# Optimization experiments

Hardware: AMD Instinct MI355X
Metric: run time of the kernel (lower is better)

The kernel has to match this reference:

```python
import jax, jax.numpy as jnp
import numpy as np

B, H, W, C = 1, 56, 56, 96
DI = 192          # d_inner = ssm_ratio * hidden_dim
N  = 16           # d_state
DR = 6            # dt_rank = ceil(96/16)
K  = 4            # cross-scan directions
MH = 384          # mlp hidden = 4*C
L  = H * W


def _ln(x, g, b):
    m = x.mean(-1, keepdims=True)
    v = ((x - m) ** 2).mean(-1, keepdims=True)
    return (x - m) * jax.lax.rsqrt(v + 1e-5) * g + b


def setup_inputs() -> dict:
    key = jax.random.key(0)
    ks = jax.random.split(key, 12)
    r = lambda i, shape, s=0.02: jax.random.normal(ks[i], shape, jnp.float32) * s
    # S4D-real init for A_logs: log(1..N) tiled over K*DI channels
    A_logs = jnp.log(jnp.tile(jnp.arange(1, N + 1, dtype=jnp.float32)[None, :], (K * DI, 1)))
    return dict(
        x=jax.random.normal(ks[0], (B, H, W, C), jnp.float32),
        norm_g=jnp.ones((C,)), norm_b=jnp.zeros((C,)),
        in_proj_w=r(1, (C, 2 * DI)),
        conv_w=r(2, (3, 3, 1, DI)), conv_b=jnp.zeros((DI,)),
        x_proj_w=r(3, (K, DR + 2 * N, DI)),
        dt_projs_w=r(4, (K, DI, DR), 0.1), dt_projs_b=r(5, (K, DI), 0.1),
        A_logs=A_logs, Ds=jnp.ones((K * DI,)),
        out_norm_g=jnp.ones((DI,)), out_norm_b=jnp.zeros((DI,)),
        out_proj_w=r(6, (DI, C)),
        norm2_g=jnp.ones((C,)), norm2_b=jnp.zeros((C,)),
        fc1_w=r(7, (C, MH)), fc1_b=jnp.zeros((MH,)),
        fc2_w=r(8, (MH, C)), fc2_b=jnp.zeros((C,)),
    )


def _ss2d(x, in_proj_w, conv_w, conv_b, x_proj_w, dt_projs_w, dt_projs_b,
          A_logs, Ds, out_norm_g, out_norm_b, out_proj_w):
    xz = x @ in_proj_w                                  # (B,H,W,2*DI)
    xx, z = xz[..., :DI], xz[..., DI:]
    z = jax.nn.silu(z)
    xx = jax.lax.conv_general_dilated(
        xx, conv_w, (1, 1), 'SAME',
        dimension_numbers=('NHWC', 'HWIO', 'NHWC'),
        feature_group_count=DI) + conv_b               # depthwise 3x3
    xx = jax.nn.silu(xx)
    # cross-scan: row-major, col-major, and their reverses -> (B,K,DI,L)
    xd = jnp.transpose(xx, (0, 3, 1, 2)).reshape(B, DI, L)
    xt = jnp.transpose(xx, (0, 3, 2, 1)).reshape(B, DI, L)
    xs = jnp.stack([xd, xt, xd[..., ::-1], xt[..., ::-1]], 1)
    xdbl = jnp.einsum('bkdl,kcd->bkcl', xs, x_proj_w)
    dts, Bs, Cs = xdbl[:, :, :DR], xdbl[:, :, DR:DR + N], xdbl[:, :, DR + N:]
    dts = jnp.einsum('bkrl,kdr->bkdl', dts, dt_projs_w)
    dts = jax.nn.softplus(dts + dt_projs_b[None, :, :, None])      # (B,K,DI,L)
    A = -jnp.exp(A_logs).reshape(K, DI, N)
    # selective scan as first-order linear recurrence h_t = a_t*h_{t-1} + b_t
    a = jnp.exp(dts[..., None] * A[None, :, :, None, :])           # (B,K,DI,L,N)
    b = dts[..., None] * jnp.swapaxes(Bs, -1, -2)[:, :, None] * xs[..., None]
    def comb(c1, c2):
        a1, b1 = c1
        a2, b2 = c2
        return a1 * a2, a2 * b1 + b2
    _, hs = jax.lax.associative_scan(comb, (a, b), axis=3)         # (B,K,DI,L,N)
    ys = jnp.einsum('bkdln,bknl->bkdl', hs, Cs) + Ds.reshape(K, DI)[None, :, :, None] * xs
    # cross-merge: un-flip, un-transpose, sum the 4 directions
    yrow = ys[:, 0] + ys[:, 2, :, ::-1]
    ycol = ys[:, 1] + ys[:, 3, :, ::-1]
    y = yrow + jnp.transpose(ycol.reshape(B, DI, W, H), (0, 1, 3, 2)).reshape(B, DI, L)
    y = jnp.transpose(y.reshape(B, DI, H, W), (0, 2, 3, 1))        # (B,H,W,DI)
    y = _ln(y, out_norm_g, out_norm_b) * z
    return y @ out_proj_w


def reference(x, norm_g, norm_b, in_proj_w, conv_w, conv_b, x_proj_w,
              dt_projs_w, dt_projs_b, A_logs, Ds, out_norm_g, out_norm_b,
              out_proj_w, norm2_g, norm2_b, fc1_w, fc1_b, fc2_w, fc2_b):
    x = x + _ss2d(_ln(x, norm_g, norm_b), in_proj_w, conv_w, conv_b, x_proj_w,
                  dt_projs_w, dt_projs_b, A_logs, Ds, out_norm_g, out_norm_b, out_proj_w)
    h = _ln(x, norm2_g, norm2_b)
    x = x + (jax.nn.gelu(h @ fc1_w + fc1_b) @ fc2_w + fc2_b)
    return x
```

## Files before the change

kernel.cpp:

```cpp
#include <hip/hip_runtime.h>
#include <math.h>

constexpr int cH = 56, cW = 56, cC = 96, cDI = 192, cN = 16, cDR = 6, cK = 4, cMH = 384;
constexpr int cL = cH * cW;
constexpr int cNC = 98;
constexpr int cCH = 32;
constexpr float LOG2E = 1.44269504088896340736f;

__device__ __forceinline__ float fast_exp2(float x) { return __builtin_amdgcn_exp2f(x); }
__device__ __forceinline__ float siluf(float x) { return x / (1.f + expf(-x)); }
__device__ __forceinline__ float geluf(float x) {
    float x3 = x * x * x;
    return 0.5f * x * (1.f + tanhf(0.7978845608028654f * (x + 0.044715f * x3)));
}

template <int ACT, bool HASB>
__global__ __launch_bounds__(256) void gemm_ln_tile(
    const float* __restrict__ A, const float* __restrict__ g, const float* __restrict__ b,
    const float* __restrict__ B, const float* __restrict__ bias,
    float* __restrict__ C, int M, int Nn) {
    __shared__ float As[64][100];
    __shared__ float Bs2[32][32];
    __shared__ float gB[96], bB[96], rowM[64], rowR[64];
    int tid = threadIdx.x;
    int row0 = blockIdx.y * 64;
    int n0 = blockIdx.x * 32;
    if (tid < 96) { gB[tid] = g[tid]; bB[tid] = b[tid]; }
#pragma unroll
    for (int t = 0; t < 6; t++) {
        int f = tid + t * 256;
        int ar = f / 24, ac4 = (f % 24) * 4;
        const float4 v = *reinterpret_cast<const float4*>(A + (size_t)(row0 + ar) * 96 + ac4);
        *reinterpret_cast<float4*>(&As[ar][ac4]) = v;
    }
    __syncthreads();
    {
        int row = tid >> 2, q = tid & 3;
        float s = 0.f, sq = 0.f;
#pragma unroll
        for (int c = 0; c < 24; c++) {
            float v = As[row][q * 24 + c];
            s += v; sq += v * v;
        }
        s += __shfl_xor(s, 1); sq += __shfl_xor(sq, 1);
        s += __shfl_xor(s, 2); sq += __shfl_xor(sq, 2);
        if (q == 0) {
            float m = s * (1.f / 96.f);
            float var = sq * (1.f / 96.f) - m * m;
            rowM[row] = m;
            rowR[row] = rsqrtf(var + 1e-5f);
        }
    }
    __syncthreads();
    for (int i = tid; i < 64 * 96; i += 256) {
        int r = i / 96, c = i % 96;
        As[r][c] = (As[r][c] - rowM[r]) * rowR[r] * gB[c] + bB[c];
    }
    __syncthreads();
    int tx = tid & 15, ty = tid >> 4;
    float acc[4][2] = {{0.f, 0.f}, {0.f, 0.f}, {0.f, 0.f}, {0.f, 0.f}};
#pragma unroll
    for (int kt = 0; kt < 3; kt++) {
        {
            int br = tid >> 3, bc = (tid & 7) * 4;
            const float4 v = *reinterpret_cast<const float4*>(
                B + (size_t)(kt * 32 + br) * Nn + n0 + bc);
            *reinterpret_cast<float4*>(&Bs2[br][bc]) = v;
        }
        __syncthreads();
#pragma unroll
        for (int k4 = 0; k4 < 8; k4++) {
            float4 a0 = *reinterpret_cast<float4*>(&As[ty * 4 + 0][kt * 32 + k4 * 4]);
            float4 a1 = *reinterpret_cast<float4*>(&As[ty * 4 + 1][kt * 32 + k4 * 4]);
            float4 a2 = *reinterpret_cast<float4*>(&As[ty * 4 + 2][kt * 32 + k4 * 4]);
            float4 a3 = *reinterpret_cast<float4*>(&As[ty * 4 + 3][kt * 32 + k4 * 4]);
            float2 b0 = *reinterpret_cast<float2*>(&Bs2[k4 * 4 + 0][tx * 2]);
            float2 b1 = *reinterpret_cast<float2*>(&Bs2[k4 * 4 + 1][tx * 2]);
            float2 b2 = *reinterpret_cast<float2*>(&Bs2[k4 * 4 + 2][tx * 2]);
            float2 b3 = *reinterpret_cast<float2*>(&Bs2[k4 * 4 + 3][tx * 2]);
            acc[0][0] = fmaf(a0.x, b0.x, acc[0][0]); acc[0][1] = fmaf(a0.x, b0.y, acc[0][1]);
            acc[1][0] = fmaf(a1.x, b0.x, acc[1][0]); acc[1][1] = fmaf(a1.x, b0.y, acc[1][1]);
            acc[2][0] = fmaf(a2.x, b0.x, acc[2][0]); acc[2][1] = fmaf(a2.x, b0.y, acc[2][1]);
            acc[3][0] = fmaf(a3.x, b0.x, acc[3][0]); acc[3][1] = fmaf(a3.x, b0.y, acc[3][1]);
            acc[0][0] = fmaf(a0.y, b1.x, acc[0][0]); acc[0][1] = fmaf(a0.y, b1.y, acc[0][1]);
            acc[1][0] = fmaf(a1.y, b1.x, acc[1][0]); acc[1][1] = fmaf(a1.y, b1.y, acc[1][1]);
            acc[2][0] = fmaf(a2.y, b1.x, acc[2][0]); acc[2][1] = fmaf(a2.y, b1.y, acc[2][1]);
            acc[3][0] = fmaf(a3.y, b1.x, acc[3][0]); acc[3][1] = fmaf(a3.y, b1.y, acc[3][1]);
            acc[0][0] = fmaf(a0.z, b2.x, acc[0][0]); acc[0][1] = fmaf(a0.z, b2.y, acc[0][1]);
            acc[1][0] = fmaf(a1.z, b2.x, acc[1][0]); acc[1][1] = fmaf(a1.z, b2.y, acc[1][1]);
            acc[2][0] = fmaf(a2.z, b2.x, acc[2][0]); acc[2][1] = fmaf(a2.z, b2.y, acc[2][1]);
            acc[3][0] = fmaf(a3.z, b2.x, acc[3][0]); acc[3][1] = fmaf(a3.z, b2.y, acc[3][1]);
            acc[0][0] = fmaf(a0.w, b3.x, acc[0][0]); acc[0][1] = fmaf(a0.w, b3.y, acc[0][1]);
            acc[1][0] = fmaf(a1.w, b3.x, acc[1][0]); acc[1][1] = fmaf(a1.w, b3.y, acc[1][1]);
            acc[2][0] = fmaf(a2.w, b3.x, acc[2][0]); acc[2][1] = fmaf(a2.w, b3.y, acc[2][1]);
            acc[3][0] = fmaf(a3.w, b3.x, acc[3][0]); acc[3][1] = fmaf(a3.w, b3.y, acc[3][1]);
        }
        __syncthreads();
    }
    int cc = n0 + tx * 2;
    float bx_ = 0.f, by_ = 0.f;
    if (HASB) { bx_ = bias[cc]; by_ = bias[cc + 1]; }
#pragma unroll
    for (int i = 0; i < 4; i++) {
        int rr = row0 + ty * 4 + i;
        float v0 = acc[i][0], v1 = acc[i][1];
        if (HASB) { v0 += bx_; v1 += by_; }
        if (ACT == 1) { v0 = geluf(v0); v1 = geluf(v1); }
        float2 o; o.x = v0; o.y = v1;
        *reinterpret_cast<float2*>(C + (size_t)rr * Nn + cc) = o;
    }
}

template <int ACT, bool HASB, bool HASR>
__global__ __launch_bounds__(256) void gemm_tile_kernel(
    const float* __restrict__ A, const float* __restrict__ B,
    const float* __restrict__ bias, const float* __restrict__ res,
    float* __restrict__ C, int M, int Nn, int Kk) {
    __shared__ float As[64][36];
    __shared__ float Bs[32][32];
    int tid = threadIdx.x;
    int tx = tid & 15;
    int ty = tid >> 4;
    int row0 = blockIdx.y * 64;
    int n0 = blockIdx.x * 32;
    float acc[4][2] = {{0.f, 0.f}, {0.f, 0.f}, {0.f, 0.f}, {0.f, 0.f}};
    int nt = Kk >> 5;
    for (int kt = 0; kt < nt; kt++) {
#pragma unroll
        for (int t = 0; t < 2; t++) {
            int f = tid + t * 256;
            int ar = f >> 3, ac = (f & 7) * 4;
            const float4 v = *reinterpret_cast<const float4*>(
                A + (size_t)(row0 + ar) * Kk + kt * 32 + ac);
            *reinterpret_cast<float4*>(&As[ar][ac]) = v;
        }
        {
            int br = tid >> 3, bc = (tid & 7) * 4;
            const float4 v = *reinterpret_cast<const float4*>(
                B + (size_t)(kt * 32 + br) * Nn + n0 + bc);
            *reinterpret_cast<float4*>(&Bs[br][bc]) = v;
        }
        __syncthreads();
#pragma unroll
        for (int k4 = 0; k4 < 8; k4++) {
            float4 a0 = *reinterpret_cast<float4*>(&As[ty * 4 + 0][k4 * 4]);
            float4 a1 = *reinterpret_cast<float4*>(&As[ty * 4 + 1][k4 * 4]);
            float4 a2 = *reinterpret_cast<float4*>(&As[ty * 4 + 2][k4 * 4]);
            float4 a3 = *reinterpret_cast<float4*>(&As[ty * 4 + 3][k4 * 4]);
            float2 b0 = *reinterpret_cast<float2*>(&Bs[k4 * 4 + 0][tx * 2]);
            float2 b1 = *reinterpret_cast<float2*>(&Bs[k4 * 4 + 1][tx * 2]);
            float2 b2 = *reinterpret_cast<float2*>(&Bs[k4 * 4 + 2][tx * 2]);
            float2 b3 = *reinterpret_cast<float2*>(&Bs[k4 * 4 + 3][tx * 2]);
            acc[0][0] = fmaf(a0.x, b0.x, acc[0][0]); acc[0][1] = fmaf(a0.x, b0.y, acc[0][1]);
            acc[1][0] = fmaf(a1.x, b0.x, acc[1][0]); acc[1][1] = fmaf(a1.x, b0.y, acc[1][1]);
            acc[2][0] = fmaf(a2.x, b0.x, acc[2][0]); acc[2][1] = fmaf(a2.x, b0.y, acc[2][1]);
            acc[3][0] = fmaf(a3.x, b0.x, acc[3][0]); acc[3][1] = fmaf(a3.x, b0.y, acc[3][1]);
            acc[0][0] = fmaf(a0.y, b1.x, acc[0][0]); acc[0][1] = fmaf(a0.y, b1.y, acc[0][1]);
            acc[1][0] = fmaf(a1.y, b1.x, acc[1][0]); acc[1][1] = fmaf(a1.y, b1.y, acc[1][1]);
            acc[2][0] = fmaf(a2.y, b1.x, acc[2][0]); acc[2][1] = fmaf(a2.y, b1.y, acc[2][1]);
            acc[3][0] = fmaf(a3.y, b1.x, acc[3][0]); acc[3][1] = fmaf(a3.y, b1.y, acc[3][1]);
            acc[0][0] = fmaf(a0.z, b2.x, acc[0][0]); acc[0][1] = fmaf(a0.z, b2.y, acc[0][1]);
            acc[1][0] = fmaf(a1.z, b2.x, acc[1][0]); acc[1][1] = fmaf(a1.z, b2.y, acc[1][1]);
            acc[2][0] = fmaf(a2.z, b2.x, acc[2][0]); acc[2][1] = fmaf(a2.z, b2.y, acc[2][1]);
            acc[3][0] = fmaf(a3.z, b2.x, acc[3][0]); acc[3][1] = fmaf(a3.z, b2.y, acc[3][1]);
            acc[0][0] = fmaf(a0.w, b3.x, acc[0][0]); acc[0][1] = fmaf(a0.w, b3.y, acc[0][1]);
            acc[1][0] = fmaf(a1.w, b3.x, acc[1][0]); acc[1][1] = fmaf(a1.w, b3.y, acc[1][1]);
            acc[2][0] = fmaf(a2.w, b3.x, acc[2][0]); acc[2][1] = fmaf(a2.w, b3.y, acc[2][1]);
            acc[3][0] = fmaf(a3.w, b3.x, acc[3][0]); acc[3][1] = fmaf(a3.w, b3.y, acc[3][1]);
        }
        __syncthreads();
    }
    int cc = n0 + tx * 2;
    float bx_ = 0.f, by_ = 0.f;
    if (HASB) { bx_ = bias[cc]; by_ = bias[cc + 1]; }
#pragma unroll
    for (int i = 0; i < 4; i++) {
        int rr = row0 + ty * 4 + i;
        float v0 = acc[i][0], v1 = acc[i][1];
        if (HASB) { v0 += bx_; v1 += by_; }
        if (ACT == 1) { v0 = geluf(v0); v1 = geluf(v1); }
        if (HASR) {
            const float2 r2 = *reinterpret_cast<const float2*>(res + (size_t)rr * Nn + cc);
            v0 += r2.x; v1 += r2.y;
        }
        float2 o; o.x = v0; o.y = v1;
        *reinterpret_cast<float2*>(C + (size_t)rr * Nn + cc) = o;
    }
}

__global__ void conv_silu_kernel(const float* __restrict__ xz, const float* __restrict__ cw,
                                 const float* __restrict__ cb, float* __restrict__ out) {
    int idx = blockIdx.x * 256 + threadIdx.x;
    if (idx >= cL * cDI) return;
    int d = idx % cDI;
    int l = idx / cDI;
    int h = l / cW, w = l % cW;
    float s = cb[d];
#pragma unroll
    for (int dh = 0; dh < 3; dh++) {
        int hh = h + dh - 1;
        if (hh < 0 || hh >= cH) continue;
#pragma unroll
        for (int dw = 0; dw < 3; dw++) {
            int w2 = w + dw - 1;
            if (w2 < 0 || w2 >= cW) continue;
            s = fmaf(xz[(size_t)(hh * cW + w2) * (2 * cDI) + d], cw[(dh * 3 + dw) * cDI + d], s);
        }
    }
    out[idx] = siluf(s);
}

__global__ void proj_kernel(const float* __restrict__ xconv, const float* __restrict__ xpw,
                            const float* __restrict__ dtw, const float* __restrict__ dtb,
                            float* __restrict__ dtT, float* __restrict__ Bsout,
                            float* __restrict__ Csout) {
    __shared__ float XS[16 * 196];
    __shared__ float DTS[6 * 16];
    __shared__ float DTW[cDI * cDR];
    int k = blockIdx.y;
    int p0 = blockIdx.x * 16;
    int tid = threadIdx.x;
    for (int i = tid; i < cDI * cDR; i += 256) DTW[i] = dtw[k * cDI * cDR + i];
    for (int idx = tid; idx < 16 * cDI; idx += 256) {
        int p = idx / cDI, d = idx % cDI;
        int j = p0 + p;
        int jj = (k >= 2) ? (cL - 1 - j) : j;
        int rrow = (k & 1) ? ((jj % cH) * cW + (jj / cH)) : jj;
        XS[p * 196 + d] = xconv[(size_t)rrow * cDI + d];
    }
    __syncthreads();
    for (int o = tid; o < 38 * 16; o += 256) {
        int c = o >> 4, p = o & 15;
        const float* wr = xpw + (size_t)(k * 38 + c) * cDI;
        const float* xr = XS + p * 196;
        float a0 = 0.f, a1 = 0.f, a2 = 0.f, a3 = 0.f;
#pragma unroll 4
        for (int d = 0; d < cDI; d += 4) {
            const float4 wv = *reinterpret_cast<const float4*>(wr + d);
            const float4 xv = *reinterpret_cast<const float4*>(xr + d);
            a0 = fmaf(wv.x, xv.x, a0);
            a1 = fmaf(wv.y, xv.y, a1);
            a2 = fmaf(wv.z, xv.z, a2);
            a3 = fmaf(wv.w, xv.w, a3);
        }
        float s = (a0 + a1) + (a2 + a3);
        if (c < 6) DTS[c * 16 + p] = s;
        else if (c < 22) Bsout[(size_t)(k * cL + p0 + p) * cN + (c - 6)] = s;
        else Csout[(size_t)(k * cL + p0 + p) * cN + (c - 22)] = s;
    }
    __syncthreads();
    for (int o = tid; o < cDI * 16; o += 256) {
        int d = o % cDI, p = o / cDI;
        float s = dtb[k * cDI + d];
#pragma unroll
        for (int r = 0; r < cDR; r++) s = fmaf(DTW[d * cDR + r], DTS[r * 16 + p], s);
        float sp = (s > 20.f) ? s : log1pf(expf(s));
        dtT[(size_t)(k * cL + p0 + p) * cDI + d] = sp;
    }
}

__device__ __forceinline__ void walker_init(int k, int j0, int& r, int& dr) {
    if (k == 0) { r = j0; dr = 1; }
    else if (k == 1) { r = (j0 % cH) * cW + (j0 / cH); dr = cW; }
    else if (k == 2) { r = cL - 1 - j0; dr = -1; }
    else { int jp = cL - 1 - j0; r = (jp % cH) * cW + (jp / cH); dr = -cW; }
}
__device__ __forceinline__ void walker_step(int& r, int dr) {
    r += dr;
    if (r >= cL) r -= cL - 1;
    else if (r < 0) r += cL - 1;
}

__global__ __launch_bounds__(192) void scan1_kernel(
    const float* __restrict__ dtT, const float* __restrict__ Bs,
    const float* __restrict__ xconv, const float* __restrict__ Alogs,
    float* __restrict__ carryP, float* __restrict__ carryH) {
    int c = blockIdx.x % cNC;
    int k = blockIdx.x / cNC;
    int d = threadIdx.x;
    int kd = k * cDI + d;
    int j0 = c * cCH;
    __shared__ float BS[cCH * cN];
    for (int i = threadIdx.x; i < cCH * cN; i += 192)
        BS[i] = Bs[(size_t)(k * cL + j0) * cN + i];
    float An2[cN];
#pragma unroll
    for (int n = 0; n < cN; n++)
        An2[n] = -fast_exp2(Alogs[kd * cN + n] * LOG2E) * LOG2E;
    int r, dr;
    walker_init(k, j0, r, dr);
    __syncthreads();
    float h[cN];
#pragma unroll
    for (int n = 0; n < cN; n++) h[n] = 0.f;
    float S = 0.f;
    const float* dtp = dtT + (size_t)(k * cL + j0) * cDI + d;
    for (int i = 0; i < cCH; i++) {
        float dt = dtp[(size_t)i * cDI];
        float xv = xconv[r * cDI + d];
        walker_step(r, dr);
        float dtx = dt * xv;
        S += dt;
        const float4 b0 = *reinterpret_cast<const float4*>(&BS[i * cN + 0]);
        const float4 b1 = *reinterpret_cast<const float4*>(&BS[i * cN + 4]);
        const float4 b2 = *reinterpret_cast<const float4*>(&BS[i * cN + 8]);
        const float4 b3 = *reinterpret_cast<const float4*>(&BS[i * cN + 12]);
        float bb[cN] = {b0.x, b0.y, b0.z, b0.w, b1.x, b1.y, b1.z, b1.w,
                        b2.x, b2.y, b2.z, b2.w, b3.x, b3.y, b3.z, b3.w};
#pragma unroll
        for (int n = 0; n < cN; n++) {
            float a = fast_exp2(An2[n] * dt);
            h[n] = fmaf(a, h[n], bb[n] * dtx);
        }
    }
    size_t cb = (size_t)(kd * cNC + c) * cN;
#pragma unroll
    for (int n = 0; n < cN; n++) {
        carryH[cb + n] = h[n];
        carryP[cb + n] = fast_exp2(An2[n] * S);
    }
}

__global__ void scan2_kernel(const float* __restrict__ carryP, const float* __restrict__ carryH,
                             float* __restrict__ hin) {
    int gid = blockIdx.x * 256 + threadIdx.x;
    if (gid >= cK * cDI * cN) return;
    int kd = gid / cN, n = gid % cN;
    float h = 0.f;
    for (int c = 0; c < cNC; c++) {
        size_t idxc = (size_t)(kd * cNC + c) * cN + n;
        hin[idxc] = h;
        h = fmaf(carryP[idxc], h, carryH[idxc]);
    }
}

__global__ __launch_bounds__(192) void scan3_kernel(
    const float* __restrict__ dtT, const float* __restrict__ Bs,
    const float* __restrict__ Cs, const float* __restrict__ xconv,
    const float* __restrict__ Alogs, const float* __restrict__ Ds,
    const float* __restrict__ hin, float* __restrict__ ysS) {
    int c = blockIdx.x % cNC;
    int k = blockIdx.x / cNC;
    int d = threadIdx.x;
    int kd = k * cDI + d;
    int j0 = c * cCH;
    __shared__ float BS[cCH * cN];
    __shared__ float CS[cCH * cN];
    for (int i = threadIdx.x; i < cCH * cN; i += 192) {
        BS[i] = Bs[(size_t)(k * cL + j0) * cN + i];
        CS[i] = Cs[(size_t)(k * cL + j0) * cN + i];
    }
    float An2[cN];
#pragma unroll
    for (int n = 0; n < cN; n++)
        An2[n] = -fast_exp2(Alogs[kd * cN + n] * LOG2E) * LOG2E;
    float Dv = Ds[kd];
    int r, dr;
    walker_init(k, j0, r, dr);
    float h[cN];
    size_t cb = (size_t)(kd * cNC + c) * cN;
#pragma unroll
    for (int n = 0; n < cN; n++) h[n] = hin[cb + n];
    __syncthreads();
    const float* dtp = dtT + (size_t)(k * cL + j0) * cDI + d;
    float* yp = ysS + (size_t)(k * cL + j0) * cDI + d;
    for (int i = 0; i < cCH; i++) {
        float dt = dtp[(size_t)i * cDI];
        float xv = xconv[r * cDI + d];
        walker_step(r, dr);
        float dtx = dt * xv;
        const float4 b0 = *reinterpret_cast<const float4*>(&BS[i * cN + 0]);
        const float4 b1 = *reinterpret_cast<const float4*>(&BS[i * cN + 4]);
        const float4 b2 = *reinterpret_cast<const float4*>(&BS[i * cN + 8]);
        const float4 b3 = *reinterpret_cast<const float4*>(&BS[i * cN + 12]);
        float bb[cN] = {b0.x, b0.y, b0.z, b0.w, b1.x, b1.y, b1.z, b1.w,
                        b2.x, b2.y, b2.z, b2.w, b3.x, b3.y, b3.z, b3.w};
        const float4 c0 = *reinterpret_cast<const float4*>(&CS[i * cN + 0]);
        const float4 c1 = *reinterpret_cast<const float4*>(&CS[i * cN + 4]);
        const float4 c2 = *reinterpret_cast<const float4*>(&CS[i * cN + 8]);
        const float4 c3 = *reinterpret_cast<const float4*>(&CS[i * cN + 12]);
        float cc[cN] = {c0.x, c0.y, c0.z, c0.w, c1.x, c1.y, c1.z, c1.w,
                        c2.x, c2.y, c2.z, c2.w, c3.x, c3.y, c3.z, c3.w};
        float y0 = 0.f, y1 = 0.f, y2 = 0.f, y3 = 0.f;
#pragma unroll
        for (int n = 0; n < cN; n += 4) {
            float a0 = fast_exp2(An2[n + 0] * dt);
            float a1 = fast_exp2(An2[n + 1] * dt);
            float a2 = fast_exp2(An2[n + 2] * dt);
            float a3 = fast_exp2(An2[n + 3] * dt);
            h[n + 0] = fmaf(a0, h[n + 0], bb[n + 0] * dtx);
            h[n + 1] = fmaf(a1, h[n + 1], bb[n + 1] * dtx);
            h[n + 2] = fmaf(a2, h[n + 2], bb[n + 2] * dtx);
            h[n + 3] = fmaf(a3, h[n + 3], bb[n + 3] * dtx);
            y0 = fmaf(h[n + 0], cc[n + 0], y0);
            y1 = fmaf(h[n + 1], cc[n + 1], y1);
            y2 = fmaf(h[n + 2], cc[n + 2], y2);
            y3 = fmaf(h[n + 3], cc[n + 3], y3);
        }
        yp[(size_t)i * cDI] = (y0 + y1) + (y2 + y3) + Dv * xv;
    }
}

__global__ void lnout_kernel(const float* __restrict__ ysS, const float* __restrict__ xz,
                             const float* __restrict__ g, const float* __restrict__ b,
                             float* __restrict__ ymul) {
    int wid = threadIdx.x >> 6, lane = threadIdx.x & 63;
    int l = blockIdx.x * 4 + wid;
    if (l >= cL) return;
    int h_ = l / cW, w_ = l % cW;
    int lc = w_ * cH + h_;
    float v[3];
    float s = 0.f, sq = 0.f;
#pragma unroll
    for (int j = 0; j < 3; j++) {
        int d = lane + j * 64;
        float t = ysS[(size_t)(0 * cL + l) * cDI + d] +
                  ysS[(size_t)(1 * cL + lc) * cDI + d] +
                  ysS[(size_t)(2 * cL + (cL - 1 - l)) * cDI + d] +
                  ysS[(size_t)(3 * cL + (cL - 1 - lc)) * cDI + d];
        v[j] = t;
        s += t;
        sq += t * t;
    }
#pragma unroll
    for (int off = 32; off; off >>= 1) {
        s += __shfl_xor(s, off, 64);
        sq += __shfl_xor(sq, off, 64);
    }
    float m = s * (1.f / cDI);
    float var = sq * (1.f / cDI) - m * m;
    float rstd = rsqrtf(var + 1e-5f);
#pragma unroll
    for (int j = 0; j < 3; j++) {
        int d = lane + j * 64;
        float z = xz[(size_t)l * (2 * cDI) + cDI + d];
        ymul[(size_t)l * cDI + d] = ((v[j] - m) * rstd * g[d] + b[d]) * siluf(z);
    }
}

extern "C" void kernel_launch(void* const* d_in, const int* in_sizes, int n_in,
                              void* d_out, int out_size, void* d_ws, size_t ws_size,
                              hipStream_t stream) {
    const float* x         = (const float*)d_in[0];
    const float* norm_g    = (const float*)d_in[1];
    const float* norm_b    = (const float*)d_in[2];
    const float* in_proj_w = (const float*)d_in[3];
    const float* conv_w    = (const float*)d_in[4];
    const float* conv_b    = (const float*)d_in[5];
    const float* x_proj_w  = (const float*)d_in[6];
    const float* dt_projs_w= (const float*)d_in[7];
    const float* dt_projs_b= (const float*)d_in[8];
    const float* A_logs    = (const float*)d_in[9];
    const float* Ds        = (const float*)d_in[10];
    const float* out_norm_g= (const float*)d_in[11];
    const float* out_norm_b= (const float*)d_in[12];
    const float* out_proj_w= (const float*)d_in[13];
    const float* norm2_g   = (const float*)d_in[14];
    const float* norm2_b   = (const float*)d_in[15];
    const float* fc1_w     = (const float*)d_in[16];
    const float* fc1_b     = (const float*)d_in[17];
    const float* fc2_w     = (const float*)d_in[18];
    const float* fc2_b     = (const float*)d_in[19];

    float* ws = (float*)d_ws;
    float* xz     = ws;
    float* xconv  = ws + 1204224;
    float* dtT    = ws + 1806336;
    float* Bs     = ws + 4214784;
    float* Cs     = ws + 4415488;
    float* hin    = ws + 4616192;
    float* cP     = ws + 5820416;
    float* cHh    = ws + 7024640;
    float* ysS    = ws + 8228864;
    float* x1     = ws + 10637312;
    float* ymul   = xconv;
    float* hm     = xz;
    float* out    = (float*)d_out;

    gemm_ln_tile<0, false><<<dim3(384 / 32, cL / 64), 256, 0, stream>>>(
        x, norm_g, norm_b, in_proj_w, nullptr, xz, cL, 2 * cDI);
    conv_silu_kernel<<<(cL * cDI) / 256, 256, 0, stream>>>(xz, conv_w, conv_b, xconv);
    proj_kernel<<<dim3(cL / 16, cK), 256, 0, stream>>>(xconv, x_proj_w, dt_projs_w,
                                                       dt_projs_b, dtT, Bs, Cs);
    scan1_kernel<<<cK * cNC, 192, 0, stream>>>(dtT, Bs, xconv, A_logs, cP, cHh);
    scan2_kernel<<<(cK * cDI * cN + 255) / 256, 256, 0, stream>>>(cP, cHh, hin);
    scan3_kernel<<<cK * cNC, 192, 0, stream>>>(dtT, Bs, Cs, xconv, A_logs, Ds, hin, ysS);
    lnout_kernel<<<cL / 4, 256, 0, stream>>>(ysS, xz, out_norm_g, out_norm_b, ymul);
    gemm_tile_kernel<0, false, true><<<dim3(96 / 32, cL / 64), 256, 0, stream>>>(
        ymul, out_proj_w, nullptr, x, x1, cL, cC, cDI);
    gemm_ln_tile<1, true><<<dim3(384 / 32, cL / 64), 256, 0, stream>>>(
        x1, norm2_g, norm2_b, fc1_w, fc1_b, hm, cL, cMH);
    gemm_tile_kernel<0, true, true><<<dim3(96 / 32, cL / 64), 256, 0, stream>>>(
        hm, fc2_w, fc2_b, x1, out, cL, cC, cMH);
}
```

Before: 163.0 us.

## Fuse projection with chunk scan, pre-permute cross-scan inputs, fuse out-norm with out_proj

The conv kernel now writes the four cross-scan orderings of its output directly, so later stages read them contiguously instead of walking strided indices. The x_proj/dt_proj kernel now also runs the first chunked scan pass on 16-step chunks from shared memory, which removes the separate scan1 launch and its re-reads of dt, B and x. Scan3 reads hin at every other chunk to match the finer chunking. The out-norm/gating kernel is fused with the out_proj GEMM plus residual, so the gated activations no longer go to global memory. The costs are four times the xs writes, twice as many carries for scan2, and a simple non-tiled GEMM in the fused out_proj.

```diff
diff --git a/kernel.cpp b/kernel.cpp
--- a/kernel.cpp
+++ b/kernel.cpp
@@ -3,8 +3,10 @@
 
 constexpr int cH = 56, cW = 56, cC = 96, cDI = 192, cN = 16, cDR = 6, cK = 4, cMH = 384;
 constexpr int cL = cH * cW;
-constexpr int cNC = 98;
-constexpr int cCH = 32;
+constexpr int cNC1 = 196;
+constexpr int cCH1 = 16;
+constexpr int cNC3 = 98;
+constexpr int cCH3 = 32;
 constexpr float LOG2E = 1.44269504088896340736f;
 
 __device__ __forceinline__ float fast_exp2(float x) { return __builtin_amdgcn_exp2f(x); }
@@ -189,7 +191,7 @@
 }
 
 __global__ void conv_silu_kernel(const float* __restrict__ xz, const float* __restrict__ cw,
-                                 const float* __restrict__ cb, float* __restrict__ out) {
+                                 const float* __restrict__ cb, float* __restrict__ xsS) {
     int idx = blockIdx.x * 256 + threadIdx.x;
     if (idx >= cL * cDI) return;
     int d = idx % cDI;
@@ -207,31 +209,38 @@
             s = fmaf(xz[(size_t)(hh * cW + w2) * (2 * cDI) + d], cw[(dh * 3 + dw) * cDI + d], s);
         }
     }
-    out[idx] = siluf(s);
-}
-
-__global__ void proj_kernel(const float* __restrict__ xconv, const float* __restrict__ xpw,
-                            const float* __restrict__ dtw, const float* __restrict__ dtb,
-                            float* __restrict__ dtT, float* __restrict__ Bsout,
-                            float* __restrict__ Csout) {
+    s = siluf(s);
+    int j1 = w * cH + h;
+    xsS[(size_t)(0 * cL + l) * cDI + d] = s;
+    xsS[(size_t)(1 * cL + j1) * cDI + d] = s;
+    xsS[(size_t)(2 * cL + (cL - 1 - l)) * cDI + d] = s;
+    xsS[(size_t)(3 * cL + (cL - 1 - j1)) * cDI + d] = s;
+}
+
+__global__ __launch_bounds__(256) void proj_scan1_kernel(
+    const float* __restrict__ xsS, const float* __restrict__ xpw,
+    const float* __restrict__ dtw, const float* __restrict__ dtb,
+    const float* __restrict__ Alogs,
+    float* __restrict__ dtT, float* __restrict__ Bsout, float* __restrict__ Csout,
+    float* __restrict__ carryP, float* __restrict__ carryH) {
     __shared__ float XS[16 * 196];
     __shared__ float DTS[6 * 16];
     __shared__ float DTW[cDI * cDR];
+    __shared__ float BSL[16 * 16];
+    __shared__ float DTL[16 * cDI];
     int k = blockIdx.y;
-    int p0 = blockIdx.x * 16;
+    int c = blockIdx.x;
+    int p0 = c * 16;
     int tid = threadIdx.x;
     for (int i = tid; i < cDI * cDR; i += 256) DTW[i] = dtw[k * cDI * cDR + i];
     for (int idx = tid; idx < 16 * cDI; idx += 256) {
         int p = idx / cDI, d = idx % cDI;
-        int j = p0 + p;
-        int jj = (k >= 2) ? (cL - 1 - j) : j;
-        int rrow = (k & 1) ? ((jj % cH) * cW + (jj / cH)) : jj;
-        XS[p * 196 + d] = xconv[(size_t)rrow * cDI + d];
+        XS[p * 196 + d] = xsS[(size_t)(k * cL + p0 + p) * cDI + d];
     }
     __syncthreads();
     for (int o = tid; o < 38 * 16; o += 256) {
-        int c = o >> 4, p = o & 15;
-        const float* wr = xpw + (size_t)(k * 38 + c) * cDI;
+        int cc = o >> 4, p = o & 15;
+        const float* wr = xpw + (size_t)(k * 38 + cc) * cDI;
         const float* xr = XS + p * 196;
         float a0 = 0.f, a1 = 0.f, a2 = 0.f, a3 = 0.f;
 #pragma unroll 4
@@ -244,9 +253,11 @@
             a3 = fmaf(wv.w, xv.w, a3);
         }
         float s = (a0 + a1) + (a2 + a3);
-        if (c < 6) DTS[c * 16 + p] = s;
-        else if (c < 22) Bsout[(size_t)(k * cL + p0 + p) * cN + (c - 6)] = s;
-        else Csout[(size_t)(k * cL + p0 + p) * cN + (c - 22)] = s;
+        if (cc < 6) DTS[cc * 16 + p] = s;
+        else if (cc < 22) {
+            BSL[p * 16 + (cc - 6)] = s;
+            Bsout[(size_t)(k * cL + p0 + p) * cN + (cc - 6)] = s;
+        } else Csout[(size_t)(k * cL + p0 + p) * cN + (cc - 22)] = s;
     }
     __syncthreads();
     for (int o = tid; o < cDI * 16; o += 256) {
@@ -255,69 +266,44 @@
 #pragma unroll
         for (int r = 0; r < cDR; r++) s = fmaf(DTW[d * cDR + r], DTS[r * 16 + p], s);
         float sp = (s > 20.f) ? s : log1pf(expf(s));
+        DTL[p * cDI + d] = sp;
         dtT[(size_t)(k * cL + p0 + p) * cDI + d] = sp;
     }
-}
-
-__device__ __forceinline__ void walker_init(int k, int j0, int& r, int& dr) {
-    if (k == 0) { r = j0; dr = 1; }
-    else if (k == 1) { r = (j0 % cH) * cW + (j0 / cH); dr = cW; }
-    else if (k == 2) { r = cL - 1 - j0; dr = -1; }
-    else { int jp = cL - 1 - j0; r = (jp % cH) * cW + (jp / cH); dr = -cW; }
-}
-__device__ __forceinline__ void walker_step(int& r, int dr) {
-    r += dr;
-    if (r >= cL) r -= cL - 1;
-    else if (r < 0) r += cL - 1;
-}
-
-__global__ __launch_bounds__(192) void scan1_kernel(
-    const float* __restrict__ dtT, const float* __restrict__ Bs,
-    const float* __restrict__ xconv, const float* __restrict__ Alogs,
-    float* __restrict__ carryP, float* __restrict__ carryH) {
-    int c = blockIdx.x % cNC;
-    int k = blockIdx.x / cNC;
-    int d = threadIdx.x;
-    int kd = k * cDI + d;
-    int j0 = c * cCH;
-    __shared__ float BS[cCH * cN];
-    for (int i = threadIdx.x; i < cCH * cN; i += 192)
-        BS[i] = Bs[(size_t)(k * cL + j0) * cN + i];
-    float An2[cN];
-#pragma unroll
-    for (int n = 0; n < cN; n++)
-        An2[n] = -fast_exp2(Alogs[kd * cN + n] * LOG2E) * LOG2E;
-    int r, dr;
-    walker_init(k, j0, r, dr);
-    __syncthreads();
-    float h[cN];
-#pragma unroll
-    for (int n = 0; n < cN; n++) h[n] = 0.f;
-    float S = 0.f;
-    const float* dtp = dtT + (size_t)(k * cL + j0) * cDI + d;
-    for (int i = 0; i < cCH; i++) {
-        float dt = dtp[(size_t)i * cDI];
-        float xv = xconv[r * cDI + d];
-        walker_step(r, dr);
-        float dtx = dt * xv;
-        S += dt;
-        const float4 b0 = *reinterpret_cast<const float4*>(&BS[i * cN + 0]);
-        const float4 b1 = *reinterpret_cast<const float4*>(&BS[i * cN + 4]);
-        const float4 b2 = *reinterpret_cast<const float4*>(&BS[i * cN + 8]);
-        const float4 b3 = *reinterpret_cast<const float4*>(&BS[i * cN + 12]);
-        float bb[cN] = {b0.x, b0.y, b0.z, b0.w, b1.x, b1.y, b1.z, b1.w,
-                        b2.x, b2.y, b2.z, b2.w, b3.x, b3.y, b3.z, b3.w};
+    __syncthreads();
+    if (tid < cDI) {
+        int d = tid;
+        int kd = k * cDI + d;
+        float An2[cN];
+#pragma unroll
+        for (int n = 0; n < cN; n++)
+            An2[n] = -fast_exp2(Alogs[kd * cN + n] * LOG2E) * LOG2E;
+        float h[cN];
+#pragma unroll
+        for (int n = 0; n < cN; n++) h[n] = 0.f;
+        float S = 0.f;
+        for (int p = 0; p < cCH1; p++) {
+            float dt = DTL[p * cDI + d];
+            float xv = XS[p * 196 + d];
+            float dtx = dt * xv;
+            S += dt;
+            const float4 b0 = *reinterpret_cast<const float4*>(&BSL[p * 16 + 0]);
+            const float4 b1 = *reinterpret_cast<const float4*>(&BSL[p * 16 + 4]);
+            const float4 b2 = *reinterpret_cast<const float4*>(&BSL[p * 16 + 8]);
+            const float4 b3 = *reinterpret_cast<const float4*>(&BSL[p * 16 + 12]);
+            float bb[cN] = {b0.x, b0.y, b0.z, b0.w, b1.x, b1.y, b1.z, b1.w,
+                            b2.x, b2.y, b2.z, b2.w, b3.x, b3.y, b3.z, b3.w};
+#pragma unroll
+            for (int n = 0; n < cN; n++) {
+                float a = fast_exp2(An2[n] * dt);
+                h[n] = fmaf(a, h[n], bb[n] * dtx);
+            }
+        }
+        size_t cb = (size_t)(kd * cNC1 + c) * cN;
 #pragma unroll
         for (int n = 0; n < cN; n++) {
-            float a = fast_exp2(An2[n] * dt);
-            h[n] = fmaf(a, h[n], bb[n] * dtx);
-        }
-    }
-    size_t cb = (size_t)(kd * cNC + c) * cN;
-#pragma unroll
-    for (int n = 0; n < cN; n++) {
-        carryH[cb + n] = h[n];
-        carryP[cb + n] = fast_exp2(An2[n] * S);
+            carryH[cb + n] = h[n];
+            carryP[cb + n] = fast_exp2(An2[n] * S);
+        }
     }
 }
 
@@ -327,8 +313,8 @@
     if (gid >= cK * cDI * cN) return;
     int kd = gid / cN, n = gid % cN;
     float h = 0.f;
-    for (int c = 0; c < cNC; c++) {
-        size_t idxc = (size_t)(kd * cNC + c) * cN + n;
+    for (int c = 0; c < cNC1; c++) {
+        size_t idxc = (size_t)(kd * cNC1 + c) * cN + n;
         hin[idxc] = h;
         h = fmaf(carryP[idxc], h, carryH[idxc]);
     }
@@ -336,17 +322,17 @@
 
 __global__ __launch_bounds__(192) void scan3_kernel(
     const float* __restrict__ dtT, const float* __restrict__ Bs,
-    const float* __restrict__ Cs, const float* __restrict__ xconv,
+    const float* __restrict__ Cs, const float* __restrict__ xsS,
     const float* __restrict__ Alogs, const float* __restrict__ Ds,
     const float* __restrict__ hin, float* __restrict__ ysS) {
-    int c = blockIdx.x % cNC;
-    int k = blockIdx.x / cNC;
+    int c3 = blockIdx.x % cNC3;
+    int k = blockIdx.x / cNC3;
     int d = threadIdx.x;
     int kd = k * cDI + d;
-    int j0 = c * cCH;
-    __shared__ float BS[cCH * cN];
-    __shared__ float CS[cCH * cN];
-    for (int i = threadIdx.x; i < cCH * cN; i += 192) {
+    int j0 = c3 * cCH3;
+    __shared__ float BS[cCH3 * cN];
+    __shared__ float CS[cCH3 * cN];
+    for (int i = threadIdx.x; i < cCH3 * cN; i += 192) {
         BS[i] = Bs[(size_t)(k * cL + j0) * cN + i];
         CS[i] = Cs[(size_t)(k * cL + j0) * cN + i];
     }
@@ -355,19 +341,17 @@
     for (int n = 0; n < cN; n++)
         An2[n] = -fast_exp2(Alogs[kd * cN + n] * LOG2E) * LOG2E;
     float Dv = Ds[kd];
-    int r, dr;
-    walker_init(k, j0, r, dr);
     float h[cN];
-    size_t cb = (size_t)(kd * cNC + c) * cN;
-#pragma unroll
-    for (int n = 0; n < cN; n++) h[n] = hin[cb + n];
+    size_t hb = (size_t)(kd * cNC1 + 2 * c3) * cN;
+#pragma unroll
+    for (int n = 0; n < cN; n++) h[n] = hin[hb + n];
     __syncthreads();
     const float* dtp = dtT + (size_t)(k * cL + j0) * cDI + d;
+    const float* xsp = xsS + (size_t)(k * cL + j0) * cDI + d;
     float* yp = ysS + (size_t)(k * cL + j0) * cDI + d;
-    for (int i = 0; i < cCH; i++) {
+    for (int i = 0; i < cCH3; i++) {
         float dt = dtp[(size_t)i * cDI];
-        float xv = xconv[r * cDI + d];
-        walker_step(r, dr);
+        float xv = xsp[(size_t)i * cDI];
         float dtx = dt * xv;
         const float4 b0 = *reinterpret_cast<const float4*>(&BS[i * cN + 0]);
         const float4 b1 = *reinterpret_cast<const float4*>(&BS[i * cN + 4]);
@@ -378,9 +362,9 @@
         const float4 c0 = *reinterpret_cast<const float4*>(&CS[i * cN + 0]);
         const float4 c1 = *reinterpret_cast<const float4*>(&CS[i * cN + 4]);
         const float4 c2 = *reinterpret_cast<const float4*>(&CS[i * cN + 8]);
-        const float4 c3 = *reinterpret_cast<const float4*>(&CS[i * cN + 12]);
+        const float4 c3v = *reinterpret_cast<const float4*>(&CS[i * cN + 12]);
         float cc[cN] = {c0.x, c0.y, c0.z, c0.w, c1.x, c1.y, c1.z, c1.w,
-                        c2.x, c2.y, c2.z, c2.w, c3.x, c3.y, c3.z, c3.w};
+                        c2.x, c2.y, c2.z, c2.w, c3v.x, c3v.y, c3v.z, c3v.w};
         float y0 = 0.f, y1 = 0.f, y2 = 0.f, y3 = 0.f;
 #pragma unroll
         for (int n = 0; n < cN; n += 4) {
@@ -401,40 +385,74 @@
     }
 }
 
-__global__ void lnout_kernel(const float* __restrict__ ysS, const float* __restrict__ xz,
-                             const float* __restrict__ g, const float* __restrict__ b,
-                             float* __restrict__ ymul) {
-    int wid = threadIdx.x >> 6, lane = threadIdx.x & 63;
-    int l = blockIdx.x * 4 + wid;
-    if (l >= cL) return;
-    int h_ = l / cW, w_ = l % cW;
-    int lc = w_ * cH + h_;
-    float v[3];
-    float s = 0.f, sq = 0.f;
-#pragma unroll
-    for (int j = 0; j < 3; j++) {
-        int d = lane + j * 64;
-        float t = ysS[(size_t)(0 * cL + l) * cDI + d] +
+__global__ __launch_bounds__(256) void lnout_proj_kernel(
+    const float* __restrict__ ysS, const float* __restrict__ xz,
+    const float* __restrict__ g, const float* __restrict__ b,
+    const float* __restrict__ W, const float* __restrict__ resx,
+    float* __restrict__ x1) {
+    __shared__ float YL[8][200];
+    __shared__ float gB[cDI], bB[cDI], rowM[8], rowR[8];
+    int tid = threadIdx.x;
+    int l0 = blockIdx.x * 8;
+    if (tid < cDI) { gB[tid] = g[tid]; bB[tid] = b[tid]; }
+#pragma unroll
+    for (int t = 0; t < 6; t++) {
+        int idx = tid + t * 256;
+        int r = idx / cDI, d = idx % cDI;
+        int l = l0 + r;
+        int h_ = l / cW, w_ = l % cW;
+        int lc = w_ * cH + h_;
+        float v = ysS[(size_t)(0 * cL + l) * cDI + d] +
                   ysS[(size_t)(1 * cL + lc) * cDI + d] +
                   ysS[(size_t)(2 * cL + (cL - 1 - l)) * cDI + d] +
                   ysS[(size_t)(3 * cL + (cL - 1 - lc)) * cDI + d];
-        v[j] = t;
-        s += t;
-        sq += t * t;
-    }
-#pragma unroll
-    for (int off = 32; off; off >>= 1) {
-        s += __shfl_xor(s, off, 64);
-        sq += __shfl_xor(sq, off, 64);
-    }
-    float m = s * (1.f / cDI);
-    float var = sq * (1.f / cDI) - m * m;
-    float rstd = rsqrtf(var + 1e-5f);
-#pragma unroll
-    for (int j = 0; j < 3; j++) {
-        int d = lane + j * 64;
+        YL[r][d] = v;
+    }
+    __syncthreads();
+    {
+        int r = tid >> 5, sg = tid & 31;
+        float s = 0.f, sq = 0.f;
+#pragma unroll
+        for (int m = 0; m < 6; m++) {
+            float v = YL[r][sg + 32 * m];
+            s += v; sq += v * v;
+        }
+        s += __shfl_xor(s, 1, 32); sq += __shfl_xor(sq, 1, 32);
+        s += __shfl_xor(s, 2, 32); sq += __shfl_xor(sq, 2, 32);
+        s += __shfl_xor(s, 4, 32); sq += __shfl_xor(sq, 4, 32);
+        s += __shfl_xor(s, 8, 32); sq += __shfl_xor(sq, 8, 32);
+        s += __shfl_xor(s, 16, 32); sq += __shfl_xor(sq, 16, 32);
+        if (sg == 0) {
+            float m = s * (1.f / cDI);
+            float var = sq * (1.f / cDI) - m * m;
+            rowM[r] = m;
+            rowR[r] = rsqrtf(var + 1e-5f);
+        }
+    }
+    __syncthreads();
+#pragma unroll
+    for (int t = 0; t < 6; t++) {
+        int idx = tid + t * 256;
+        int r = idx / cDI, d = idx % cDI;
+        int l = l0 + r;
         float z = xz[(size_t)l * (2 * cDI) + cDI + d];
-        ymul[(size_t)l * cDI + d] = ((v[j] - m) * rstd * g[d] + b[d]) * siluf(z);
+        YL[r][d] = ((YL[r][d] - rowM[r]) * rowR[r] * gB[d] + bB[d]) * siluf(z);
+    }
+    __syncthreads();
+#pragma unroll
+    for (int t = 0; t < 3; t++) {
+        int o = tid + t * 256;
+        int r = o / 96, cc = o % 96;
+        float a0 = 0.f, a1 = 0.f, a2 = 0.f, a3 = 0.f;
+#pragma unroll 4
+        for (int kk = 0; kk < cDI; kk += 4) {
+            a0 = fmaf(YL[r][kk + 0], W[(size_t)(kk + 0) * 96 + cc], a0);
+            a1 = fmaf(YL[r][kk + 1], W[(size_t)(kk + 1) * 96 + cc], a1);
+            a2 = fmaf(YL[r][kk + 2], W[(size_t)(kk + 2) * 96 + cc], a2);
+            a3 = fmaf(YL[r][kk + 3], W[(size_t)(kk + 3) * 96 + cc], a3);
+        }
+        int l = l0 + r;
+        x1[(size_t)l * 96 + cc] = (a0 + a1) + (a2 + a3) + resx[(size_t)l * 96 + cc];
     }
 }
 
@@ -464,30 +482,27 @@
 
     float* ws = (float*)d_ws;
     float* xz     = ws;
-    float* xconv  = ws + 1204224;
-    float* dtT    = ws + 1806336;
-    float* Bs     = ws + 4214784;
-    float* Cs     = ws + 4415488;
-    float* hin    = ws + 4616192;
-    float* cP     = ws + 5820416;
-    float* cHh    = ws + 7024640;
-    float* ysS    = ws + 8228864;
-    float* x1     = ws + 10637312;
-    float* ymul   = xconv;
+    float* xsS    = ws + 1204224;
+    float* dtT    = ws + 3612672;
+    float* Bs     = ws + 6021120;
+    float* Cs     = ws + 6221824;
+    float* cP     = ws + 6422528;
+    float* cHh    = ws + 8830976;
+    float* hin    = ws + 11239424;
+    float* ysS    = ws + 13647872;
+    float* x1     = ws + 16056320;
     float* hm     = xz;
     float* out    = (float*)d_out;
 
     gemm_ln_tile<0, false><<<dim3(384 / 32, cL / 64), 256, 0, stream>>>(
         x, norm_g, norm_b, in_proj_w, nullptr, xz, cL, 2 * cDI);
-    conv_silu_kernel<<<(cL * cDI) / 256, 256, 0, stream>>>(xz, conv_w, conv_b, xconv);
-    proj_kernel<<<dim3(cL / 16, cK), 256, 0, stream>>>(xconv, x_proj_w, dt_projs_w,
-                                                       dt_projs_b, dtT, Bs, Cs);
-    scan1_kernel<<<cK * cNC, 192, 0, stream>>>(dtT, Bs, xconv, A_logs, cP, cHh);
+    conv_silu_kernel<<<(cL * cDI) / 256, 256, 0, stream>>>(xz, conv_w, conv_b, xsS);
+    proj_scan1_kernel<<<dim3(cNC1, cK), 256, 0, stream>>>(
+        xsS, x_proj_w, dt_projs_w, dt_projs_b, A_logs, dtT, Bs, Cs, cP, cHh);
     scan2_kernel<<<(cK * cDI * cN + 255) / 256, 256, 0, stream>>>(cP, cHh, hin);
-    scan3_kernel<<<cK * cNC, 192, 0, stream>>>(dtT, Bs, Cs, xconv, A_logs, Ds, hin, ysS);
-    lnout_kernel<<<cL / 4, 256, 0, stream>>>(ysS, xz, out_norm_g, out_norm_b, ymul);
-    gemm_tile_kernel<0, false, true><<<dim3(96 / 32, cL / 64), 256, 0, stream>>>(
-        ymul, out_proj_w, nullptr, x, x1, cL, cC, cDI);
+    scan3_kernel<<<cK * cNC3, 192, 0, stream>>>(dtT, Bs, Cs, xsS, A_logs, Ds, hin, ysS);
+    lnout_proj_kernel<<<cL / 8, 256, 0, stream>>>(ysS, xz, out_norm_g, out_norm_b,
+                                                  out_proj_w, x, x1);
     gemm_ln_tile<1, true><<<dim3(384 / 32, cL / 64), 256, 0, stream>>>(
         x1, norm2_g, norm2_b, fc1_w, fc1_b, hm, cL, cMH);
     gemm_tile_kernel<0, true, true><<<dim3(96 / 32, cL / 64), 256, 0, stream>>>(
```

New measurement: 162.4 us. No clear change (-0.4%).
